# Performance work log

Hardware: AMD Instinct MI355X
Metric: run time of the kernel (lower is better)

Reference implementation:

```python
import jax, jax.numpy as jnp
import numpy as np

T, B, D, L, C, H = 100, 4096, 32, 32, 64, 128  # steps, batch, state_dim, latent, context, hidden


def setup_inputs() -> dict:
    key = jax.random.key(0)
    ks = jax.random.split(key, 32)
    def rn(k, shape, scale=0.1):
        return jax.random.normal(k, shape, dtype=jnp.float32) * scale
    return dict(
        xs=rn(ks[0], (T, B, D), 1.0),
        ts=jnp.arange(T, dtype=jnp.float32) * 0.01,
        eps0=rn(ks[1], (B, L), 1.0),
        noise=rn(ks[2], (T - 1, B, L), 1.0),
        gru_Wih=rn(ks[3], (3 * H, D)), gru_Whh=rn(ks[4], (3 * H, H)),
        gru_bih=rn(ks[5], (3 * H,)), gru_bhh=rn(ks[6], (3 * H,)),
        enc_W=rn(ks[7], (C, H)), enc_b=rn(ks[8], (C,)),
        qz0_W=rn(ks[9], (2 * L, C)), qz0_b=rn(ks[10], (2 * L,)),
        fW1=rn(ks[11], (H, L + C)), fb1=rn(ks[12], (H,)),
        fW2=rn(ks[13], (H, H)), fb2=rn(ks[14], (H,)),
        fW3=rn(ks[15], (L, H)), fb3=rn(ks[16], (L,)),
        hW1=rn(ks[17], (H, L)), hb1=rn(ks[18], (H,)),
        hW2=rn(ks[19], (H, H)), hb2=rn(ks[20], (H,)),
        hW3=rn(ks[21], (L, H)), hb3=rn(ks[22], (L,)),
        gW1=rn(ks[23], (L, H)), gb1=rn(ks[24], (L, H)),
        gW2=rn(ks[25], (L, H)), gb2=rn(ks[26], (L,)),
        projW=rn(ks[27], (D, L)), projb=rn(ks[28], (D,)),
    )


def reference(xs, ts, eps0, noise, gru_Wih, gru_Whh, gru_bih, gru_bhh,
              enc_W, enc_b, qz0_W, qz0_b,
              fW1, fb1, fW2, fb2, fW3, fb3,
              hW1, hb1, hW2, hb2, hW3, hb3,
              gW1, gb1, gW2, gb2, projW, projb):
    sp = jax.nn.softplus

    # --- Encoder: GRU (PyTorch gate order r,z,n) + Linear ---
    def gru_step(h, x):
        gi = x @ gru_Wih.T + gru_bih
        gh = h @ gru_Whh.T + gru_bhh
        ir, iz, inn = jnp.split(gi, 3, axis=-1)
        hr, hz, hn = jnp.split(gh, 3, axis=-1)
        r = jax.nn.sigmoid(ir + hr)
        z = jax.nn.sigmoid(iz + hz)
        n = jnp.tanh(inn + r * hn)
        h = (1.0 - z) * n + z * h
        return h, h

    h0 = jnp.zeros((xs.shape[1], gru_Whh.shape[1]), xs.dtype)
    _, hs = jax.lax.scan(gru_step, h0, xs)          # [T,B,H]
    ctx = hs @ enc_W.T + enc_b                      # [T,B,C]

    # --- posterior z0 ---
    qz0 = ctx[0] @ qz0_W.T + qz0_b
    mean, logstd = jnp.split(qz0, 2, axis=-1)
    z0 = mean + jnp.exp(logstd) * eps0              # [B,L]

    def f_mlp(x):  # posterior drift f_net
        return sp(sp(x @ fW1.T + fb1) @ fW2.T + fb2) @ fW3.T + fb3

    def h_mlp(y):  # prior drift h_net
        return sp(sp(y @ hW1.T + hb1) @ hW2.T + hb2) @ hW3.T + hb3

    def diag_g(y):  # batched per-dim 1->H->1 sigmoid MLPs (the g_nets loop)
        hmid = sp(y[..., None] * gW1 + gb1)          # [B,L,H]
        return jax.nn.sigmoid(jnp.sum(hmid * gW2, -1) + gb2)  # [B,L]

    dts = ts[1:] - ts[:-1]

    def sde_step(carry, inp):
        y, lq = carry
        c, dt, dW = inp
        f = f_mlp(jnp.concatenate([y, c], axis=-1))
        hdr = h_mlp(y)
        g = diag_g(y)
        u = (f - hdr) / g                            # KL path-wise term
        lq = lq + 0.5 * jnp.sum(u * u, axis=-1) * dt
        y = y + f * dt + g * jnp.sqrt(dt) * dW       # Euler-Maruyama
        return (y, lq), y

    (zT, logqp), ys = jax.lax.scan(
        sde_step, (z0, jnp.zeros(z0.shape[0], z0.dtype)), (ctx[:-1], dts, noise))
    zs = jnp.concatenate([z0[None], ys], axis=0)     # [T,B,L]
    xs_hat = zs @ projW.T + projb                    # [T,B,D]
    return xs_hat, logqp
```

## Files before the change

### kernel.cpp

```cpp
#include <hip/hip_runtime.h>


#define TT 100
#define BB 4096
#define DD 32
#define LL 32
#define CC 64
#define HH 128
#define GROW 260

typedef _Float16 h1;
typedef _Float16 h2 __attribute__((ext_vector_type(2)));
typedef _Float16 f16x8 __attribute__((ext_vector_type(8)));
typedef float f32x4 __attribute__((ext_vector_type(4)));

#define MFMA(a, b, c) __builtin_amdgcn_mfma_f32_16x16x32_f16(a, b, c, 0, 0, 0)
#define PIN(x) asm volatile("" : "+v"(x))

__device__ __forceinline__ void bar_lds() {
  __builtin_amdgcn_sched_barrier(0);
  asm volatile("s_waitcnt lgkmcnt(0)" ::: "memory");
  __builtin_amdgcn_s_barrier();
  asm volatile("" ::: "memory");
  __builtin_amdgcn_sched_barrier(0);
}

__device__ __forceinline__ float sigm(float x) {
  return 1.0f / (1.0f + __expf(-x));
}
__device__ __forceinline__ float tanh_(float x) {
  float e = __expf(2.0f * fminf(x, 15.0f));
  return (e - 1.0f) / (e + 1.0f);
}
__device__ __forceinline__ float splus(float x) {
  return __logf(1.0f + __expf(x));
}

__device__ __forceinline__ f16x8 bfrag(const float* __restrict__ W, int K,
                                       int n0, int k0, int lane) {
  const float* p = W + (size_t)(n0 + (lane & 15)) * K + k0 + ((lane >> 4) << 3);
  f16x8 r;
#pragma unroll
  for (int j = 0; j < 8; ++j) r[j] = (h1)p[j];
  return r;
}

__device__ __forceinline__ f16x8 afrag(const h1* base, int ld, int k0,
                                       int lane) {
  return *(const f16x8*)(base + (size_t)(lane & 15) * ld + k0 +
                         ((lane >> 4) << 3));
}

__device__ __forceinline__ void store_swz(h1* base, const float* __restrict__ W,
                                          int rows, int tid, int nthr) {
  for (int idx = tid; idx < rows * 64; idx += nthr) {
    const int n = idx >> 6, kp = idx & 63;
    float2 v = *(const float2*)(W + (size_t)n * HH + 2 * kp);
    h2 hv;
    hv[0] = (h1)v.x;
    hv[1] = (h1)v.y;
    int byte = n * 256 + kp * 4;
    byte ^= (n & 7) << 4;
    *(h2*)((char*)base + byte) = hv;
  }
}
__device__ __forceinline__ f16x8 swzfrag(const h1* base, int n0, int kt,
                                         int lane) {
  const int n = n0 + (lane & 15);
  int byte = n * 256 + kt * 64 + ((lane >> 4) << 4);
  byte ^= (n & 7) << 4;
  return *(const f16x8*)((const char*)base + byte);
}

__global__ __launch_bounds__(320) void k_gtab(
    const float* __restrict__ gW1, const float* __restrict__ gb1,
    const float* __restrict__ gW2, const float* __restrict__ gb2,
    float* __restrict__ gtab) {
  const int l = blockIdx.x;
  const int e = threadIdx.x;
  if (e >= 257) return;
  const float yv = -12.f + (float)e * (24.f / 256.f);
  const float* w1 = gW1 + l * HH;
  const float* bb = gb1 + l * HH;
  const float* w2 = gW2 + l * HH;
  float a = 0.f;
#pragma unroll 4
  for (int h = 0; h < HH; ++h)
    a = fmaf(splus(fmaf(yv, w1[h], bb[h])), w2[h], a);
  gtab[l * GROW + e] = sigm(a + gb2[l]);
}

__global__ __launch_bounds__(512, 2) void k_gru(
    const float* __restrict__ xs, const float* __restrict__ Wih,
    const float* __restrict__ Whh, const float* __restrict__ bih,
    const float* __restrict__ bhh, const float* __restrict__ encW,
    const float* __restrict__ encb, h1* __restrict__ ctx16) {
  __shared__ alignas(16) h1 sH[2][16][136];
  __shared__ alignas(16) h1 sX[2][16][40];
  __shared__ alignas(16) h1 sE[64 * 128];

  const int tid = threadIdx.x;
  const int lane = tid & 63, w = tid >> 6;
  const int b0 = blockIdx.x * 16;
  const int coln = lane & 15, row4 = (lane >> 4) << 2;

  f16x8 wIH[3], wHH[3][4];
#pragma unroll
  for (int g = 0; g < 3; ++g) {
    wIH[g] = bfrag(Wih, DD, 128 * g + 16 * w, 0, lane);
#pragma unroll
    for (int kt = 0; kt < 4; ++kt)
      wHH[g][kt] = bfrag(Whh, HH, 128 * g + 16 * w, 32 * kt, lane);
  }
  const int m = 16 * w + coln;
  const float b_r = bih[m] + bhh[m];
  const float b_z = bih[128 + m] + bhh[128 + m];
  const float b_ni = bih[256 + m];
  const float b_nh = bhh[256 + m];
  const int ccE = (w >= 4) ? 16 * (w - 4) + coln : 0;
  const float bE = (w >= 4) ? encb[ccE] : 0.f;

  store_swz(sE, encW, 64, tid, 512);
  for (int i = tid; i < 16 * 136; i += 512) (&sH[0][0][0])[i] = (h1)0.0f;
  sX[0][tid >> 5][tid & 31] = (h1)xs[(size_t)b0 * DD + tid];
  float xHold = xs[(size_t)1 * BB * DD + (size_t)b0 * DD + tid];
  float hold[4] = {0.f, 0.f, 0.f, 0.f};
  __syncthreads();

  for (int t = 0; t < TT; ++t) {
    const int cur = t & 1;
    const int tf = (t + 2 < TT) ? (t + 2) : (TT - 1);
    const float xFly = xs[(size_t)tf * BB * DD + (size_t)b0 * DD + tid];

#pragma unroll
    for (int g = 0; g < 3; ++g) {
      PIN(wIH[g]);
#pragma unroll
      for (int kt = 0; kt < 4; ++kt) PIN(wHH[g][kt]);
    }

    f16x8 ax = afrag(&sX[cur][0][0], 40, 0, lane);
    f32x4 aR{b_r, b_r, b_r, b_r}, aZ{b_z, b_z, b_z, b_z};
    f32x4 aNI{b_ni, b_ni, b_ni, b_ni}, aNH{b_nh, b_nh, b_nh, b_nh};
    aR = MFMA(ax, wIH[0], aR);
    aZ = MFMA(ax, wIH[1], aZ);
    aNI = MFMA(ax, wIH[2], aNI);
#pragma unroll
    for (int kt = 0; kt < 4; ++kt) {
      f16x8 ah = afrag(&sH[cur][0][0], 136, 32 * kt, lane);
      aR = MFMA(ah, wHH[0][kt], aR);
      aZ = MFMA(ah, wHH[1][kt], aZ);
      aNH = MFMA(ah, wHH[2][kt], aNH);
    }
#pragma unroll
    for (int j = 0; j < 4; ++j) {
      float rg = sigm(aR[j]);
      float zg = sigm(aZ[j]);
      float ng = tanh_(aNI[j] + rg * aNH[j]);
      float hn = (1.0f - zg) * ng + zg * hold[j];
      hold[j] = hn;
      sH[cur ^ 1][row4 + j][m] = (h1)hn;
    }
    sX[cur ^ 1][tid >> 5][tid & 31] = (h1)xHold;
    bar_lds();

    if (w >= 4) {
      f32x4 aE{bE, bE, bE, bE};
#pragma unroll
      for (int kt = 0; kt < 4; ++kt)
        aE = MFMA(afrag(&sH[cur ^ 1][0][0], 136, 32 * kt, lane),
                  swzfrag(sE, 16 * (w - 4), kt, lane), aE);
#pragma unroll
      for (int j = 0; j < 4; ++j)
        ctx16[((size_t)t * BB + b0 + row4 + j) * CC + ccE] = (h1)aE[j];
    }
    xHold = xFly;
  }
}

__global__ __launch_bounds__(512, 2) void k_sde(
    const float* __restrict__ ts, const float* __restrict__ eps0,
    const float* __restrict__ noise, const float* __restrict__ qz0W,
    const float* __restrict__ qz0b, const float* __restrict__ fW1,
    const float* __restrict__ fb1, const float* __restrict__ fW2,
    const float* __restrict__ fb2, const float* __restrict__ fW3,
    const float* __restrict__ fb3, const float* __restrict__ hW1,
    const float* __restrict__ hb1, const float* __restrict__ hW2,
    const float* __restrict__ hb2, const float* __restrict__ hW3,
    const float* __restrict__ hb3, const float* __restrict__ projW,
    const float* __restrict__ projb, const float* __restrict__ gtab,
    const h1* __restrict__ ctx16, float* __restrict__ out) {
  __shared__ alignas(16) h1 sC[16][72];
  __shared__ alignas(16) h1 sY16[16][40];
  __shared__ alignas(16) h1 sA1[16][136], sB1[16][136];
  __shared__ alignas(16) h1 sA2[16][136], sB2[16][136];
  __shared__ alignas(16) h1 sW3f[32 * 128], sW3h[32 * 128];
  __shared__ float sG[32][GROW];
  __shared__ float sDt[128], sSq[128];
  __shared__ float sTmp[16][33];

  const int tid = threadIdx.x;
  const int lane = tid & 63, w = tid >> 6;
  const int b0 = blockIdx.x * 16;
  const int coln = lane & 15, row4 = (lane >> 4) << 2;
  const bool isF = (w < 4);
  const int t2 = isF ? w : (w - 4);
  const int colA = 32 * t2 + coln, colB = colA + 16;

  f16x8 wL1a[3], wL1b[3], wL2a[4], wL2b[4], wPj;
  if (isF) {
#pragma unroll
    for (int kt = 0; kt < 3; ++kt) {
      wL1a[kt] = bfrag(fW1, 96, 32 * t2, 32 * kt, lane);
      wL1b[kt] = bfrag(fW1, 96, 32 * t2 + 16, 32 * kt, lane);
    }
#pragma unroll
    for (int kt = 0; kt < 4; ++kt) {
      wL2a[kt] = bfrag(fW2, HH, 32 * t2, 32 * kt, lane);
      wL2b[kt] = bfrag(fW2, HH, 32 * t2 + 16, 32 * kt, lane);
    }
  } else {
    wL1a[0] = bfrag(hW1, 32, 32 * t2, 0, lane);
    wL1b[0] = bfrag(hW1, 32, 32 * t2 + 16, 0, lane);
#pragma unroll
    for (int kt = 0; kt < 4; ++kt) {
      wL2a[kt] = bfrag(hW2, HH, 32 * t2, 32 * kt, lane);
      wL2b[kt] = bfrag(hW2, HH, 32 * t2 + 16, 32 * kt, lane);
    }
  }
  const float bL1a = isF ? fb1[colA] : hb1[colA];
  const float bL1b = isF ? fb1[colB] : hb1[colB];
  const float bL2a = isF ? fb2[colA] : hb2[colA];
  const float bL2b = isF ? fb2[colB] : hb2[colB];

  float bF3 = 0.f, bH3 = 0.f, bPj = 0.f;
  int cu = 0, ccp = 0, srow = 0, scol = 0;
  if (w == 4 || w == 5) {
    cu = 16 * (w - 4) + coln;
    bF3 = fb3[cu];
    bH3 = hb3[cu];
  } else if (w >= 6) {
    ccp = 16 * (w - 6) + coln;
    wPj = bfrag(projW, LL, 16 * (w - 6), 0, lane);
    bPj = projb[ccp];
    const int sidx = tid - 384;
    srow = sidx >> 3;
    scol = (sidx & 7) * 8;
  }

  store_swz(sW3f, fW3, 32, tid, 512);
  store_swz(sW3h, hW3, 32, tid, 512);
  for (int i = tid; i < 32 * GROW; i += 512) (&sG[0][0])[i] = gtab[i];
  if (tid < TT - 1) {
    float d = ts[tid + 1] - ts[tid];
    sDt[tid] = d;
    sSq[tid] = __fsqrt_rn(d);
  }
  *(h2*)&sC[tid >> 5][2 * (tid & 31)] =
      *(const h2*)(ctx16 + (size_t)(b0 + (tid >> 5)) * CC + 2 * (tid & 31));
  __syncthreads();

  {
    const int sr = tid >> 5, sc = tid & 31;
    float m0 = qz0b[sc], s0 = qz0b[32 + sc];
    const float* qm = qz0W + sc * 64;
    const float* qs = qz0W + (32 + sc) * 64;
#pragma unroll 4
    for (int k = 0; k < 64; ++k) {
      float cv = (float)sC[sr][k];
      m0 = fmaf(qm[k], cv, m0);
      s0 = fmaf(qs[k], cv, s0);
    }
    float z = fmaf(__expf(s0), eps0[(size_t)(b0 + sr) * LL + sc], m0);
    sTmp[sr][sc] = z;
    sY16[sr][sc] = (h1)z;
  }
  f16x8 cHold;
  if (w >= 6)
    cHold = *(const f16x8*)(ctx16 + ((size_t)1 * BB + b0 + srow) * CC + scol);
  float nHold[4] = {0.f, 0.f, 0.f, 0.f};
  if (w == 4 || w == 5) {
#pragma unroll
    for (int j = 0; j < 4; ++j)
      nHold[j] = noise[(size_t)(b0 + row4 + j) * LL + cu];
  }
  __syncthreads();

  float yreg[4] = {0.f, 0.f, 0.f, 0.f}, lq[4] = {0.f, 0.f, 0.f, 0.f};
  if (w == 4 || w == 5) {
#pragma unroll
    for (int j = 0; j < 4; ++j) yreg[j] = sTmp[row4 + j][cu];
  }

  f32x4 accA{bL1a, bL1a, bL1a, bL1a}, accB{bL1b, bL1b, bL1b, bL1b};
  if (isF) {
    f16x8 c0 = afrag(&sC[0][0], 72, 0, lane);
    f16x8 c1 = afrag(&sC[0][0], 72, 32, lane);
    accA = MFMA(c0, wL1a[1], accA);
    accA = MFMA(c1, wL1a[2], accA);
    accB = MFMA(c0, wL1b[1], accB);
    accB = MFMA(c1, wL1b[2], accB);
  }

  for (int t = 0; t < TT - 1; ++t) {
    f16x8 cFly;
    if (w >= 6) {
      const int tc = (t + 2 <= TT - 1) ? t + 2 : TT - 1;
      cFly = *(const f16x8*)(ctx16 + ((size_t)tc * BB + b0 + srow) * CC + scol);
    }
    float nFly[4];
    if (w == 4 || w == 5) {
      const int tn = (t + 1 < TT - 1) ? t + 1 : TT - 2;
#pragma unroll
      for (int j = 0; j < 4; ++j)
        nFly[j] = noise[((size_t)tn * BB + b0 + row4 + j) * LL + cu];
    }

    if (isF) {
#pragma unroll
      for (int kt = 0; kt < 3; ++kt) {
        PIN(wL1a[kt]);
        PIN(wL1b[kt]);
      }
    } else {
      PIN(wL1a[0]);
      PIN(wL1b[0]);
    }
#pragma unroll
    for (int kt = 0; kt < 4; ++kt) {
      PIN(wL2a[kt]);
      PIN(wL2b[kt]);
    }
    if (w >= 6) PIN(wPj);

    f16x8 aY = afrag(&sY16[0][0], 40, 0, lane);
    if (isF) {
      accA = MFMA(aY, wL1a[0], accA);
      accB = MFMA(aY, wL1b[0], accB);
#pragma unroll
      for (int j = 0; j < 4; ++j) {
        sA1[row4 + j][colA] = (h1)splus(accA[j]);
        sA1[row4 + j][colB] = (h1)splus(accB[j]);
      }
    } else {
      f32x4 hA{bL1a, bL1a, bL1a, bL1a}, hB{bL1b, bL1b, bL1b, bL1b};
      hA = MFMA(aY, wL1a[0], hA);
      hB = MFMA(aY, wL1b[0], hB);
#pragma unroll
      for (int j = 0; j < 4; ++j) {
        sB1[row4 + j][colA] = (h1)splus(hA[j]);
        sB1[row4 + j][colB] = (h1)splus(hB[j]);
      }
    }
    bar_lds();

    {
      const h1* src = isF ? &sA1[0][0] : &sB1[0][0];
      h1* dst = isF ? &sA2[0][0] : &sB2[0][0];
      f32x4 pA{bL2a, bL2a, bL2a, bL2a}, pB{bL2b, bL2b, bL2b, bL2b};
#pragma unroll
      for (int kt = 0; kt < 4; ++kt) {
        f16x8 a = afrag(src, 136, 32 * kt, lane);
        pA = MFMA(a, wL2a[kt], pA);
        pB = MFMA(a, wL2b[kt], pB);
      }
#pragma unroll
      for (int j = 0; j < 4; ++j) {
        dst[(size_t)(row4 + j) * 136 + colA] = (h1)splus(pA[j]);
        dst[(size_t)(row4 + j) * 136 + colB] = (h1)splus(pB[j]);
      }
    }
    if (w >= 6) {
      *(f16x8*)&sC[srow][scol] = cHold;
      cHold = cFly;
    }
    bar_lds();

    if (isF) {
      f16x8 c0 = afrag(&sC[0][0], 72, 0, lane);
      f16x8 c1 = afrag(&sC[0][0], 72, 32, lane);
      accA = f32x4{bL1a, bL1a, bL1a, bL1a};
      accB = f32x4{bL1b, bL1b, bL1b, bL1b};
      accA = MFMA(c0, wL1a[1], accA);
      accA = MFMA(c1, wL1a[2], accA);
      accB = MFMA(c0, wL1b[1], accB);
      accB = MFMA(c1, wL1b[2], accB);
    } else if (w < 6) {
      f32x4 aF{bF3, bF3, bF3, bF3}, aH{bH3, bH3, bH3, bH3};
#pragma unroll
      for (int kt = 0; kt < 4; ++kt) {
        aF = MFMA(afrag(&sA2[0][0], 136, 32 * kt, lane),
                  swzfrag(sW3f, 16 * (w - 4), kt, lane), aF);
        aH = MFMA(afrag(&sB2[0][0], 136, 32 * kt, lane),
                  swzfrag(sW3h, 16 * (w - 4), kt, lane), aH);
      }
      const float dtv = sDt[t], sqdt = sSq[t];
      const float* g = sG[cu];
#pragma unroll
      for (int j = 0; j < 4; ++j) {
        float p = fminf(fmaxf(fmaf(yreg[j], 32.f / 3.f, 128.f), 0.f), 255.999f);
        const int i = (int)p;
        const float fr = p - (float)i;
        const float gv = fmaf(g[i + 1] - g[i], fr, g[i]);
        const float uv = (aF[j] - aH[j]) / gv;
        lq[j] = fmaf(0.5f * uv * uv, dtv, lq[j]);
        yreg[j] = fmaf(aF[j], dtv, yreg[j]) + gv * sqdt * nHold[j];
        sY16[row4 + j][cu] = (h1)yreg[j];
      }
#pragma unroll
      for (int j = 0; j < 4; ++j) nHold[j] = nFly[j];
    } else {
      f32x4 ap{bPj, bPj, bPj, bPj};
      ap = MFMA(aY, wPj, ap);
#pragma unroll
      for (int j = 0; j < 4; ++j)
        out[((size_t)t * BB + b0 + row4 + j) * DD + ccp] = ap[j];
    }
    bar_lds();
  }

  if (w >= 6) {
    f16x8 aYf = afrag(&sY16[0][0], 40, 0, lane);
    f32x4 ap{bPj, bPj, bPj, bPj};
    ap = MFMA(aYf, wPj, ap);
#pragma unroll
    for (int j = 0; j < 4; ++j)
      out[((size_t)(TT - 1) * BB + b0 + row4 + j) * DD + ccp] = ap[j];
  }
  if (w == 4 || w == 5) {
#pragma unroll
    for (int j = 0; j < 4; ++j) sTmp[row4 + j][cu] = lq[j];
  }
  __syncthreads();
  if (tid < 16) {
    float s = 0.f;
#pragma unroll
    for (int k = 0; k < 32; ++k) s += sTmp[tid][k];
    out[(size_t)TT * BB * DD + b0 + tid] = s;
  }
}

extern "C" void kernel_launch(void* const* d_in, const int* in_sizes, int n_in,
                              void* d_out, int out_size, void* d_ws,
                              size_t ws_size, hipStream_t stream) {
  const float* xs = (const float*)d_in[0];
  const float* ts = (const float*)d_in[1];
  const float* eps0 = (const float*)d_in[2];
  const float* noise = (const float*)d_in[3];
  const float* Wih = (const float*)d_in[4];
  const float* Whh = (const float*)d_in[5];
  const float* bih = (const float*)d_in[6];
  const float* bhh = (const float*)d_in[7];
  const float* encW = (const float*)d_in[8];
  const float* encb = (const float*)d_in[9];
  const float* qz0W = (const float*)d_in[10];
  const float* qz0b = (const float*)d_in[11];
  const float* fW1 = (const float*)d_in[12];
  const float* fb1 = (const float*)d_in[13];
  const float* fW2 = (const float*)d_in[14];
  const float* fb2 = (const float*)d_in[15];
  const float* fW3 = (const float*)d_in[16];
  const float* fb3 = (const float*)d_in[17];
  const float* hW1 = (const float*)d_in[18];
  const float* hb1 = (const float*)d_in[19];
  const float* hW2 = (const float*)d_in[20];
  const float* hb2 = (const float*)d_in[21];
  const float* hW3 = (const float*)d_in[22];
  const float* hb3 = (const float*)d_in[23];
  const float* gW1 = (const float*)d_in[24];
  const float* gb1 = (const float*)d_in[25];
  const float* gW2 = (const float*)d_in[26];
  const float* gb2 = (const float*)d_in[27];
  const float* projW = (const float*)d_in[28];
  const float* projb = (const float*)d_in[29];
  float* out = (float*)d_out;
  h1* ctx16 = (h1*)d_out;
  float* gtab = (float*)d_ws;

  k_gtab<<<32, 320, 0, stream>>>(gW1, gb1, gW2, gb2, gtab);
  k_gru<<<256, 512, 0, stream>>>(xs, Wih, Whh, bih, bhh, encW, encb, ctx16);
  k_sde<<<256, 512, 0, stream>>>(ts, eps0, noise, qz0W, qz0b, fW1, fb1, fW2,
                                 fb2, fW3, fb3, hW1, hb1, hW2, hb2, hW3, hb3,
                                 projW, projb, gtab, ctx16, out);
}
```

Measured before the change: 347.3 us.

## Fuse GRU encoder into SDE kernel, pipelining context through LDS

Merges the GRU encoder and SDE integration kernels into one kernel that runs the GRU one step ahead of the SDE step in the same loop. Context vectors are passed through double-buffered shared memory instead of a global fp16 scratch buffer, which removes a kernel launch and the global ctx round-trip. In exchange, per-thread register pressure goes up a lot because GRU and MLP weights are both held in registers, and shared memory use grows. Both can reduce occupancy or cause spills.

```diff
diff --git a/kernel.cpp b/kernel.cpp
--- a/kernel.cpp
+++ b/kernel.cpp
@@ -90,14 +90,32 @@
   gtab[l * GROW + e] = sigm(a + gb2[l]);
 }
 
-__global__ __launch_bounds__(512, 2) void k_gru(
-    const float* __restrict__ xs, const float* __restrict__ Wih,
-    const float* __restrict__ Whh, const float* __restrict__ bih,
-    const float* __restrict__ bhh, const float* __restrict__ encW,
-    const float* __restrict__ encb, h1* __restrict__ ctx16) {
-  __shared__ alignas(16) h1 sH[2][16][136];
+__global__ __launch_bounds__(512, 2) void k_fused(
+    const float* __restrict__ xs, const float* __restrict__ ts,
+    const float* __restrict__ eps0, const float* __restrict__ noise,
+    const float* __restrict__ Wih, const float* __restrict__ Whh,
+    const float* __restrict__ bih, const float* __restrict__ bhh,
+    const float* __restrict__ encW, const float* __restrict__ encb,
+    const float* __restrict__ qz0W, const float* __restrict__ qz0b,
+    const float* __restrict__ fW1, const float* __restrict__ fb1,
+    const float* __restrict__ fW2, const float* __restrict__ fb2,
+    const float* __restrict__ fW3, const float* __restrict__ fb3,
+    const float* __restrict__ hW1, const float* __restrict__ hb1,
+    const float* __restrict__ hW2, const float* __restrict__ hb2,
+    const float* __restrict__ hW3, const float* __restrict__ hb3,
+    const float* __restrict__ projW, const float* __restrict__ projb,
+    const float* __restrict__ gtab, float* __restrict__ out) {
+  __shared__ alignas(16) h1 sHb[2][16][136];
   __shared__ alignas(16) h1 sX[2][16][40];
   __shared__ alignas(16) h1 sE[64 * 128];
+  __shared__ alignas(16) h1 sCtx[2][16][72];
+  __shared__ alignas(16) h1 sY16[16][40];
+  __shared__ alignas(16) h1 sA1[16][136], sB1[16][136];
+  __shared__ alignas(16) h1 sA2[16][136], sB2[16][136];
+  __shared__ alignas(16) h1 sW3f[32 * 128], sW3h[32 * 128];
+  __shared__ float sG[32][GROW];
+  __shared__ float sDt[128], sSq[128];
+  __shared__ float sTmp[16][33];
 
   const int tid = threadIdx.x;
   const int lane = tid & 63, w = tid >> 6;
@@ -120,93 +138,9 @@
   const int ccE = (w >= 4) ? 16 * (w - 4) + coln : 0;
   const float bE = (w >= 4) ? encb[ccE] : 0.f;
 
-  store_swz(sE, encW, 64, tid, 512);
-  for (int i = tid; i < 16 * 136; i += 512) (&sH[0][0][0])[i] = (h1)0.0f;
-  sX[0][tid >> 5][tid & 31] = (h1)xs[(size_t)b0 * DD + tid];
-  float xHold = xs[(size_t)1 * BB * DD + (size_t)b0 * DD + tid];
-  float hold[4] = {0.f, 0.f, 0.f, 0.f};
-  __syncthreads();
-
-  for (int t = 0; t < TT; ++t) {
-    const int cur = t & 1;
-    const int tf = (t + 2 < TT) ? (t + 2) : (TT - 1);
-    const float xFly = xs[(size_t)tf * BB * DD + (size_t)b0 * DD + tid];
-
-#pragma unroll
-    for (int g = 0; g < 3; ++g) {
-      PIN(wIH[g]);
-#pragma unroll
-      for (int kt = 0; kt < 4; ++kt) PIN(wHH[g][kt]);
-    }
-
-    f16x8 ax = afrag(&sX[cur][0][0], 40, 0, lane);
-    f32x4 aR{b_r, b_r, b_r, b_r}, aZ{b_z, b_z, b_z, b_z};
-    f32x4 aNI{b_ni, b_ni, b_ni, b_ni}, aNH{b_nh, b_nh, b_nh, b_nh};
-    aR = MFMA(ax, wIH[0], aR);
-    aZ = MFMA(ax, wIH[1], aZ);
-    aNI = MFMA(ax, wIH[2], aNI);
-#pragma unroll
-    for (int kt = 0; kt < 4; ++kt) {
-      f16x8 ah = afrag(&sH[cur][0][0], 136, 32 * kt, lane);
-      aR = MFMA(ah, wHH[0][kt], aR);
-      aZ = MFMA(ah, wHH[1][kt], aZ);
-      aNH = MFMA(ah, wHH[2][kt], aNH);
-    }
-#pragma unroll
-    for (int j = 0; j < 4; ++j) {
-      float rg = sigm(aR[j]);
-      float zg = sigm(aZ[j]);
-      float ng = tanh_(aNI[j] + rg * aNH[j]);
-      float hn = (1.0f - zg) * ng + zg * hold[j];
-      hold[j] = hn;
-      sH[cur ^ 1][row4 + j][m] = (h1)hn;
-    }
-    sX[cur ^ 1][tid >> 5][tid & 31] = (h1)xHold;
-    bar_lds();
-
-    if (w >= 4) {
-      f32x4 aE{bE, bE, bE, bE};
-#pragma unroll
-      for (int kt = 0; kt < 4; ++kt)
-        aE = MFMA(afrag(&sH[cur ^ 1][0][0], 136, 32 * kt, lane),
-                  swzfrag(sE, 16 * (w - 4), kt, lane), aE);
-#pragma unroll
-      for (int j = 0; j < 4; ++j)
-        ctx16[((size_t)t * BB + b0 + row4 + j) * CC + ccE] = (h1)aE[j];
-    }
-    xHold = xFly;
-  }
-}
-
-__global__ __launch_bounds__(512, 2) void k_sde(
-    const float* __restrict__ ts, const float* __restrict__ eps0,
-    const float* __restrict__ noise, const float* __restrict__ qz0W,
-    const float* __restrict__ qz0b, const float* __restrict__ fW1,
-    const float* __restrict__ fb1, const float* __restrict__ fW2,
-    const float* __restrict__ fb2, const float* __restrict__ fW3,
-    const float* __restrict__ fb3, const float* __restrict__ hW1,
-    const float* __restrict__ hb1, const float* __restrict__ hW2,
-    const float* __restrict__ hb2, const float* __restrict__ hW3,
-    const float* __restrict__ hb3, const float* __restrict__ projW,
-    const float* __restrict__ projb, const float* __restrict__ gtab,
-    const h1* __restrict__ ctx16, float* __restrict__ out) {
-  __shared__ alignas(16) h1 sC[16][72];
-  __shared__ alignas(16) h1 sY16[16][40];
-  __shared__ alignas(16) h1 sA1[16][136], sB1[16][136];
-  __shared__ alignas(16) h1 sA2[16][136], sB2[16][136];
-  __shared__ alignas(16) h1 sW3f[32 * 128], sW3h[32 * 128];
-  __shared__ float sG[32][GROW];
-  __shared__ float sDt[128], sSq[128];
-  __shared__ float sTmp[16][33];
-
-  const int tid = threadIdx.x;
-  const int lane = tid & 63, w = tid >> 6;
-  const int b0 = blockIdx.x * 16;
-  const int coln = lane & 15, row4 = (lane >> 4) << 2;
   const bool isF = (w < 4);
   const int t2 = isF ? w : (w - 4);
   const int colA = 32 * t2 + coln, colB = colA + 16;
-
   f16x8 wL1a[3], wL1b[3], wL2a[4], wL2b[4], wPj;
   if (isF) {
 #pragma unroll
@@ -234,7 +168,7 @@
   const float bL2b = isF ? fb2[colB] : hb2[colB];
 
   float bF3 = 0.f, bH3 = 0.f, bPj = 0.f;
-  int cu = 0, ccp = 0, srow = 0, scol = 0;
+  int cu = 0, ccp = 0;
   if (w == 4 || w == 5) {
     cu = 16 * (w - 4) + coln;
     bF3 = fb3[cu];
@@ -243,11 +177,9 @@
     ccp = 16 * (w - 6) + coln;
     wPj = bfrag(projW, LL, 16 * (w - 6), 0, lane);
     bPj = projb[ccp];
-    const int sidx = tid - 384;
-    srow = sidx >> 3;
-    scol = (sidx & 7) * 8;
-  }
-
+  }
+
+  store_swz(sE, encW, 64, tid, 512);
   store_swz(sW3f, fW3, 32, tid, 512);
   store_swz(sW3h, hW3, 32, tid, 512);
   for (int i = tid; i < 32 * GROW; i += 512) (&sG[0][0])[i] = gtab[i];
@@ -256,9 +188,49 @@
     sDt[tid] = d;
     sSq[tid] = __fsqrt_rn(d);
   }
-  *(h2*)&sC[tid >> 5][2 * (tid & 31)] =
-      *(const h2*)(ctx16 + (size_t)(b0 + (tid >> 5)) * CC + 2 * (tid & 31));
+  for (int i = tid; i < 16 * 136; i += 512) (&sHb[0][0][0])[i] = (h1)0.0f;
+  sX[0][tid >> 5][tid & 31] = (h1)xs[(size_t)b0 * DD + tid];
+  float xHold = xs[(size_t)BB * DD + (size_t)b0 * DD + tid];
+  float hold[4] = {0.f, 0.f, 0.f, 0.f};
   __syncthreads();
+
+  {
+    f16x8 ax = afrag(&sX[0][0][0], 40, 0, lane);
+    f32x4 aR{b_r, b_r, b_r, b_r}, aZ{b_z, b_z, b_z, b_z};
+    f32x4 aNI{b_ni, b_ni, b_ni, b_ni}, aNH{b_nh, b_nh, b_nh, b_nh};
+    aR = MFMA(ax, wIH[0], aR);
+    aZ = MFMA(ax, wIH[1], aZ);
+    aNI = MFMA(ax, wIH[2], aNI);
+#pragma unroll
+    for (int kt = 0; kt < 4; ++kt) {
+      f16x8 ah = afrag(&sHb[0][0][0], 136, 32 * kt, lane);
+      aR = MFMA(ah, wHH[0][kt], aR);
+      aZ = MFMA(ah, wHH[1][kt], aZ);
+      aNH = MFMA(ah, wHH[2][kt], aNH);
+    }
+#pragma unroll
+    for (int j = 0; j < 4; ++j) {
+      float rg = sigm(aR[j]);
+      float zg = sigm(aZ[j]);
+      float ng = tanh_(aNI[j] + rg * aNH[j]);
+      float hn = (1.0f - zg) * ng + zg * hold[j];
+      hold[j] = hn;
+      sHb[1][row4 + j][m] = (h1)hn;
+    }
+    sX[1][tid >> 5][tid & 31] = (h1)xHold;
+    xHold = xs[(size_t)2 * BB * DD + (size_t)b0 * DD + tid];
+  }
+  bar_lds();
+  if (w >= 4) {
+    f32x4 aE{bE, bE, bE, bE};
+#pragma unroll
+    for (int kt = 0; kt < 4; ++kt)
+      aE = MFMA(afrag(&sHb[1][0][0], 136, 32 * kt, lane),
+                swzfrag(sE, 16 * (w - 4), kt, lane), aE);
+#pragma unroll
+    for (int j = 0; j < 4; ++j) sCtx[0][row4 + j][ccE] = (h1)aE[j];
+  }
+  bar_lds();
 
   {
     const int sr = tid >> 5, sc = tid & 31;
@@ -267,7 +239,7 @@
     const float* qs = qz0W + (32 + sc) * 64;
 #pragma unroll 4
     for (int k = 0; k < 64; ++k) {
-      float cv = (float)sC[sr][k];
+      float cv = (float)sCtx[0][sr][k];
       m0 = fmaf(qm[k], cv, m0);
       s0 = fmaf(qs[k], cv, s0);
     }
@@ -275,27 +247,22 @@
     sTmp[sr][sc] = z;
     sY16[sr][sc] = (h1)z;
   }
-  f16x8 cHold;
-  if (w >= 6)
-    cHold = *(const f16x8*)(ctx16 + ((size_t)1 * BB + b0 + srow) * CC + scol);
+  __syncthreads();
+
+  float yreg[4] = {0.f, 0.f, 0.f, 0.f}, lq[4] = {0.f, 0.f, 0.f, 0.f};
   float nHold[4] = {0.f, 0.f, 0.f, 0.f};
   if (w == 4 || w == 5) {
 #pragma unroll
-    for (int j = 0; j < 4; ++j)
+    for (int j = 0; j < 4; ++j) {
+      yreg[j] = sTmp[row4 + j][cu];
       nHold[j] = noise[(size_t)(b0 + row4 + j) * LL + cu];
-  }
-  __syncthreads();
-
-  float yreg[4] = {0.f, 0.f, 0.f, 0.f}, lq[4] = {0.f, 0.f, 0.f, 0.f};
-  if (w == 4 || w == 5) {
-#pragma unroll
-    for (int j = 0; j < 4; ++j) yreg[j] = sTmp[row4 + j][cu];
+    }
   }
 
   f32x4 accA{bL1a, bL1a, bL1a, bL1a}, accB{bL1b, bL1b, bL1b, bL1b};
   if (isF) {
-    f16x8 c0 = afrag(&sC[0][0], 72, 0, lane);
-    f16x8 c1 = afrag(&sC[0][0], 72, 32, lane);
+    f16x8 c0 = afrag(&sCtx[0][0][0], 72, 0, lane);
+    f16x8 c1 = afrag(&sCtx[0][0][0], 72, 32, lane);
     accA = MFMA(c0, wL1a[1], accA);
     accA = MFMA(c1, wL1a[2], accA);
     accB = MFMA(c0, wL1b[1], accB);
@@ -303,11 +270,9 @@
   }
 
   for (int t = 0; t < TT - 1; ++t) {
-    f16x8 cFly;
-    if (w >= 6) {
-      const int tc = (t + 2 <= TT - 1) ? t + 2 : TT - 1;
-      cFly = *(const f16x8*)(ctx16 + ((size_t)tc * BB + b0 + srow) * CC + scol);
-    }
+    const int cur = t & 1;
+    const int tf = (t + 3 < TT) ? (t + 3) : (TT - 1);
+    const float xFly = xs[(size_t)tf * BB * DD + (size_t)b0 * DD + tid];
     float nFly[4];
     if (w == 4 || w == 5) {
       const int tn = (t + 1 < TT - 1) ? t + 1 : TT - 2;
@@ -316,6 +281,12 @@
         nFly[j] = noise[((size_t)tn * BB + b0 + row4 + j) * LL + cu];
     }
 
+#pragma unroll
+    for (int g = 0; g < 3; ++g) {
+      PIN(wIH[g]);
+#pragma unroll
+      for (int kt = 0; kt < 4; ++kt) PIN(wHH[g][kt]);
+    }
     if (isF) {
 #pragma unroll
       for (int kt = 0; kt < 3; ++kt) {
@@ -334,6 +305,30 @@
     if (w >= 6) PIN(wPj);
 
     f16x8 aY = afrag(&sY16[0][0], 40, 0, lane);
+    {
+      f16x8 ax = afrag(&sX[cur ^ 1][0][0], 40, 0, lane);
+      f32x4 aR{b_r, b_r, b_r, b_r}, aZ{b_z, b_z, b_z, b_z};
+      f32x4 aNI{b_ni, b_ni, b_ni, b_ni}, aNH{b_nh, b_nh, b_nh, b_nh};
+      aR = MFMA(ax, wIH[0], aR);
+      aZ = MFMA(ax, wIH[1], aZ);
+      aNI = MFMA(ax, wIH[2], aNI);
+#pragma unroll
+      for (int kt = 0; kt < 4; ++kt) {
+        f16x8 ah = afrag(&sHb[cur ^ 1][0][0], 136, 32 * kt, lane);
+        aR = MFMA(ah, wHH[0][kt], aR);
+        aZ = MFMA(ah, wHH[1][kt], aZ);
+        aNH = MFMA(ah, wHH[2][kt], aNH);
+      }
+#pragma unroll
+      for (int j = 0; j < 4; ++j) {
+        float rg = sigm(aR[j]);
+        float zg = sigm(aZ[j]);
+        float ng = tanh_(aNI[j] + rg * aNH[j]);
+        float hn = (1.0f - zg) * ng + zg * hold[j];
+        hold[j] = hn;
+        sHb[cur][row4 + j][m] = (h1)hn;
+      }
+    }
     if (isF) {
       accA = MFMA(aY, wL1a[0], accA);
       accB = MFMA(aY, wL1b[0], accB);
@@ -352,6 +347,7 @@
         sB1[row4 + j][colB] = (h1)splus(hB[j]);
       }
     }
+    sX[cur][tid >> 5][tid & 31] = (h1)xHold;
     bar_lds();
 
     {
@@ -370,15 +366,20 @@
         dst[(size_t)(row4 + j) * 136 + colB] = (h1)splus(pB[j]);
       }
     }
-    if (w >= 6) {
-      *(f16x8*)&sC[srow][scol] = cHold;
-      cHold = cFly;
+    if (w >= 4) {
+      f32x4 aE{bE, bE, bE, bE};
+#pragma unroll
+      for (int kt = 0; kt < 4; ++kt)
+        aE = MFMA(afrag(&sHb[cur][0][0], 136, 32 * kt, lane),
+                  swzfrag(sE, 16 * (w - 4), kt, lane), aE);
+#pragma unroll
+      for (int j = 0; j < 4; ++j) sCtx[cur ^ 1][row4 + j][ccE] = (h1)aE[j];
     }
     bar_lds();
 
     if (isF) {
-      f16x8 c0 = afrag(&sC[0][0], 72, 0, lane);
-      f16x8 c1 = afrag(&sC[0][0], 72, 32, lane);
+      f16x8 c0 = afrag(&sCtx[cur ^ 1][0][0], 72, 0, lane);
+      f16x8 c1 = afrag(&sCtx[cur ^ 1][0][0], 72, 32, lane);
       accA = f32x4{bL1a, bL1a, bL1a, bL1a};
       accB = f32x4{bL1b, bL1b, bL1b, bL1b};
       accA = MFMA(c0, wL1a[1], accA);
@@ -417,6 +418,7 @@
         out[((size_t)t * BB + b0 + row4 + j) * DD + ccp] = ap[j];
     }
     bar_lds();
+    xHold = xFly;
   }
 
   if (w >= 6) {
@@ -474,12 +476,11 @@
   const float* projW = (const float*)d_in[28];
   const float* projb = (const float*)d_in[29];
   float* out = (float*)d_out;
-  h1* ctx16 = (h1*)d_out;
   float* gtab = (float*)d_ws;
 
   k_gtab<<<32, 320, 0, stream>>>(gW1, gb1, gW2, gb2, gtab);
-  k_gru<<<256, 512, 0, stream>>>(xs, Wih, Whh, bih, bhh, encW, encb, ctx16);
-  k_sde<<<256, 512, 0, stream>>>(ts, eps0, noise, qz0W, qz0b, fW1, fb1, fW2,
-                                 fb2, fW3, fb3, hW1, hb1, hW2, hb2, hW3, hb3,
-                                 projW, projb, gtab, ctx16, out);
-}
+  k_fused<<<256, 512, 0, stream>>>(xs, ts, eps0, noise, Wih, Whh, bih, bhh,
+                                   encW, encb, qz0W, qz0b, fW1, fb1, fW2, fb2,
+                                   fW3, fb3, hW1, hb1, hW2, hb2, hW3, hb3,
+                                   projW, projb, gtab, out);
+}
```

After: 382.7 us. 1.1x slower.
